# Optimization experiments

Measured on AMD Instinct MI355X. Metric: run time of the kernel, lower is better.

## Reference

```python
import jax, jax.numpy as jnp
import numpy as np

# ---- fixed architecture constants (hard-coded in Wavenet_Barebones.__init__) ----
B = 2
T_FRAMES = 64
UPS = (4, 4, 4, 4)
T = T_FRAMES * 256            # 16384 audio samples
VOCAB = 259
CH = 128
CC = 80                       # conditioning (mel) channels
K = 3                         # dilated conv kernel size
LAYERS = 24
LAYERS_PER_STACK = 6          # 24 // 4
FC1 = 512


def setup_inputs() -> dict:
    key = jax.random.key(0)
    ks = iter(jax.random.split(key, 32))
    nrm = lambda shape, s: jax.random.normal(next(ks), shape, jnp.float32) * s
    return {
        "x": jax.random.randint(next(ks), (B, T), 0, VOCAB),          # mu-law token ids
        "c": jax.random.normal(next(ks), (B, CC, T_FRAMES), jnp.float32),  # mel frames (B,C,Tf)
        "emb": nrm((VOCAB, CH), 1.0),
        "enc_w": nrm((CH, CH), 0.08), "enc_b": jnp.zeros((CH,), jnp.float32),
        "conv_w": nrm((LAYERS, CH, CH, K), 0.05),  # (L, out, in, k)
        "conv_b": jnp.zeros((LAYERS, CH), jnp.float32),
        "cond_w": nrm((LAYERS, CH, CC), 0.05),     # per-layer 1x1 local-conditioning proj
        "cond_b": jnp.zeros((LAYERS, CH), jnp.float32),
        "fc1_w": nrm((FC1, CH), 0.08), "fc1_b": jnp.zeros((FC1,), jnp.float32),
        "fc2_w": nrm((VOCAB, FC1), 0.04), "fc2_b": jnp.zeros((VOCAB,), jnp.float32),
        "ups_w": nrm((4, 3, 4), 0.3),              # 4 ConvTranspose2d kernels (freq=3, time=4)
        "ups_b": jnp.zeros((4,), jnp.float32),
    }


def _upsample(c, ups_w, ups_b):
    """r9y9 UpsampleNetwork: stack of ConvTranspose2d(1,1,(3,s),stride=(1,s),padding=(1,0)) + ReLU.
    c: (B, CC, Tf) -> (B, CC, Tf*256)."""
    y = c[:, None]  # (B, 1, CC, Tf)
    for i, s in enumerate(UPS):
        # transposed conv == input dilation by s + correlation with spatially-flipped kernel
        w = ups_w[i][::-1, ::-1][None, None]  # (O=1, I=1, 3, s)
        y = jax.lax.conv_general_dilated(
            y, w, window_strides=(1, 1),
            padding=[(1, 1), (s - 1, s - 1)],   # freq: kh-1-pad=1; time: kw-1-0=s-1
            lhs_dilation=(1, s),
            dimension_numbers=("NCHW", "OIHW", "NCHW"))
        y = jax.nn.relu(y + ups_b[i])
    return y[:, 0]  # (B, CC, T)


def reference(x, c, emb, enc_w, enc_b, conv_w, conv_b, cond_w, cond_b,
              fc1_w, fc1_b, fc2_w, fc2_b, ups_w, ups_b):
    # encode: embedding -> relu(linear)   (dropout is inference-disabled)
    h = jax.nn.relu(jnp.einsum("btc,oc->bto", emb[x], enc_w) + enc_b)  # (B,T,CH)
    cu = _upsample(c, ups_w, ups_b)                                     # (B,CC,T)
    h = h.transpose(0, 2, 1)                                            # (B,CH,T)
    dn = ("NCH", "OIH", "NCH")
    for l in range(LAYERS):
        d = 2 ** (l % LAYERS_PER_STACK)
        p = (K - 1) * d  # causal left pad
        y = jax.lax.conv_general_dilated(
            h, conv_w[l], window_strides=(1,), padding=[(p, 0)],
            rhs_dilation=(d,), dimension_numbers=dn)
        y = jax.nn.relu(y + conv_b[l][:, None])
        cond = jnp.einsum("oc,bct->bot", cond_w[l], cu) + cond_b[l][:, None]
        h = jax.nn.relu(y + cond + h)  # conditioning + residual, outer F.relu from forward loop
    h = h.transpose(0, 2, 1)                                            # (B,T,CH)
    h = jax.nn.relu(jnp.einsum("btc,oc->bto", h, fc1_w) + fc1_b)
    out = jnp.einsum("btf,of->bto", h, fc2_w) + fc2_b                   # (B,T,VOCAB)
    return out[:, :-1, :]
```

## Files before the change

kernel.cpp:

```cpp
#include <hip/hip_runtime.h>

typedef __bf16 bf16;
typedef __attribute__((ext_vector_type(8))) __bf16 bf16x8;
typedef __attribute__((ext_vector_type(4))) __bf16 bf16x4;
typedef __attribute__((ext_vector_type(4))) float f32x4;

namespace {
constexpr int Bn = 2;
constexpr int T  = 16384;
constexpr int NL = 24;
constexpr int VOC = 259;
}

#define MFMA_B16(a, b, c) __builtin_amdgcn_mfma_f32_16x16x32_bf16((a), (b), (c), 0, 0, 0)

__global__ void prep_wconv_k(const float* __restrict__ cw, const float* __restrict__ dw,
                             bf16* __restrict__ W2) {
  int total = NL * 61440;
  for (int idx = blockIdx.x * 256 + threadIdx.x; idx < total; idx += gridDim.x * 256) {
    int l = idx / 61440; int r = idx % 61440;
    int s = r >> 12; int of = (r >> 9) & 7; int lane = (r >> 3) & 63; int j = r & 7;
    int o = of * 16 + (lane & 15);
    int kk = (lane >> 4) * 8 + j;
    float v;
    if (s < 12) { int k = s >> 2; int c = (s & 3) * 32 + kk; v = cw[((l * 128 + o) * 128 + c) * 3 + k]; }
    else        { int cc = (s - 12) * 32 + kk; v = (cc < 80) ? dw[(l * 128 + o) * 80 + cc] : 0.f; }
    W2[idx] = (bf16)v;
  }
}

__global__ void prep_misc_k(const float* __restrict__ fc1w, const float* __restrict__ encw,
                            const float* __restrict__ emb, const float* __restrict__ fc2w,
                            bf16* __restrict__ fc1wb, bf16* __restrict__ encwb,
                            bf16* __restrict__ embb, bf16* __restrict__ w2f) {
  const int n1 = 65536, n2 = 16384, n3 = 33152, n4 = 196608;
  int total = n1 + n2 + n3 + n4;
  for (int idx = blockIdx.x * 256 + threadIdx.x; idx < total; idx += gridDim.x * 256) {
    if (idx < n1) { fc1wb[idx] = (bf16)fc1w[idx]; }
    else if (idx < n1 + n2) { int i = idx - n1; encwb[i] = (bf16)encw[i]; }
    else if (idx < n1 + n2 + n3) { int i = idx - n1 - n2; embb[i] = (bf16)emb[i]; }
    else {
      int r = idx - n1 - n2 - n3;
      int s = r / 12288; int r2 = r % 12288;
      int ot = r2 >> 9; int lane = (r2 >> 3) & 63; int j = r2 & 7;
      int o = ot * 16 + (lane & 15);
      int f = s * 32 + (lane >> 4) * 8 + j;
      w2f[r] = (bf16)((o < VOC) ? fc2w[o * 512 + f] : 0.f);
    }
  }
}

__global__ void ups_stage_k(const float* __restrict__ in, float* __restrict__ out,
                            const float* __restrict__ W, const float* __restrict__ bptr, int Win) {
  int Wout = Win * 4;
  int total = Bn * 80 * Wout;
  float bias = *bptr;
  for (int idx = blockIdx.x * 256 + threadIdx.x; idx < total; idx += gridDim.x * 256) {
    int w = idx % Wout; int rest = idx / Wout;
    int hrow = rest % 80; int b = rest / 80;
    int win = w >> 2; int kw = w & 3;
    float acc = bias;
#pragma unroll
    for (int kh = 0; kh < 3; ++kh) {
      int hr = hrow + 1 - kh;
      if (hr >= 0 && hr < 80) acc += in[(b * 80 + hr) * Win + win] * W[kh * 4 + kw];
    }
    out[idx] = fmaxf(acc, 0.f);
  }
}

__global__ void ups4_cuT_k(const float* __restrict__ in, const float* __restrict__ W,
                           const float* __restrict__ bptr, bf16* __restrict__ cuT2) {
  int total = Bn * 1024 * 3 * 512;
  float bias = *bptr;
  for (int idx = blockIdx.x * 256 + threadIdx.x; idx < total; idx += gridDim.x * 256) {
    int low = idx & 511; int j = low & 7; int lane = low >> 3;
    int g = idx >> 9; int sc = g % 3; int gt = g / 3; int tile = gt & 1023; int b = gt >> 10;
    int lr = lane & 15, lk = lane >> 4;
    int t = tile * 16 + lr;
    int cc = sc * 32 + lk * 8 + j;
    float v = 0.f;
    if (cc < 80) {
      int win = t >> 2, kw = t & 3;
      float acc = bias;
#pragma unroll
      for (int kh = 0; kh < 3; ++kh) {
        int hr = cc + 1 - kh;
        if (hr >= 0 && hr < 80) acc += in[(b * 80 + hr) * 4096 + win] * W[kh * 4 + kw];
      }
      v = fmaxf(acc, 0.f);
    }
    cuT2[idx] = (bf16)v;
  }
}

__global__ __launch_bounds__(256, 2) void encode_k(
    const int* __restrict__ x, const bf16* __restrict__ embb, const bf16* __restrict__ encwb,
    const float* __restrict__ encb, bf16* __restrict__ hbt) {
  __shared__ char Eb[16384];
  int t0 = blockIdx.x * 64, b = blockIdx.y;
  int tid = threadIdx.x, lane = tid & 63, wid = tid >> 6, wr = wid >> 1, wc = wid & 1;
  int lr = lane & 15, lk = lane >> 4;
  int tb = t0 + wc * 32;
  int xi[2];
#pragma unroll
  for (int n = 0; n < 2; ++n) xi[n] = x[b * T + tb + n * 16 + lr];
  f32x4 acc[4][2] = {};
#pragma unroll
  for (int s = 0; s < 4; ++s) {
    bf16x8 a[4], bb[2];
#pragma unroll
    for (int m = 0; m < 4; ++m) a[m] = *(const bf16x8*)(encwb + (wr * 64 + m * 16 + lr) * 128 + s * 32 + lk * 8);
#pragma unroll
    for (int n = 0; n < 2; ++n) bb[n] = *(const bf16x8*)(embb + xi[n] * 128 + s * 32 + lk * 8);
#pragma unroll
    for (int m = 0; m < 4; ++m)
#pragma unroll
      for (int n = 0; n < 2; ++n) acc[m][n] = MFMA_B16(a[m], bb[n], acc[m][n]);
  }
#pragma unroll
  for (int m = 0; m < 4; ++m)
#pragma unroll
    for (int n = 0; n < 2; ++n) {
      int obase = wr * 64 + m * 16 + lk * 4;
      int row = wc * 32 + n * 16 + lr;
      bf16x4 p;
#pragma unroll
      for (int r = 0; r < 4; ++r) p[r] = (bf16)fmaxf(acc[m][n][r] + encb[obase + r], 0.f);
      int byteo = obase * 2;
      int slot = ((byteo >> 4) ^ (row & 7)) & 15;
      *(bf16x4*)(Eb + row * 256 + (slot << 4) + (byteo & 15)) = p;
    }
  __syncthreads();
  const size_t btb = (size_t)b * T;
  for (int u = tid; u < 1024; u += 256) {
    int row = u >> 4, slot = u & 15;
    uint4 v = *(const uint4*)(Eb + row * 256 + ((((slot) ^ (row & 7)) & 15) << 4));
    *(uint4*)(hbt + (btb + t0 + row) * 128 + slot * 8) = v;
  }
}

template <int D1>
__global__ __launch_bounds__(512, 4) void layer2_k(
    const bf16* __restrict__ hbt_in, bf16* __restrict__ hbt_out,
    const bf16* __restrict__ W2, const bf16* __restrict__ cuT2,
    const float* __restrict__ cb1, const float* __restrict__ db1,
    const float* __restrict__ cb2, const float* __restrict__ db2) {
  constexpr int D2 = 2 * D1;
  constexpr int EXT = (D1 == 16) ? 64 : 16;
  constexpr int NMF = EXT / 16;
  constexpr int NF = NMF + 4;
  constexpr int NCH = (D1 == 16) ? 2 : 1;
  constexpr int NFC = NF / NCH;
  constexpr int AOFF = EXT + 2 * D1;
  constexpr int AR = 64 + AOFF;
  constexpr int BR = 64 + EXT;
  __shared__ uint4 Au[AR * 16];
  __shared__ uint4 Bu[BR * 16];
  char* AB = (char*)Au;
  char* BB = (char*)Bu;
  const int bx = blockIdx.x;
  const int tblk = ((bx & 7) << 5) | (bx >> 3);
  const int t0 = tblk * 64, b = blockIdx.y;
  const int tid = threadIdx.x, lane = tid & 63, wid = tid >> 6;
  const int lr = lane & 15, lk = lane >> 4;
  const size_t btb = (size_t)b * T;
  const size_t bt16 = (size_t)b * 1024;
  const bf16* Wa = W2;
  const bf16* Wb = W2 + 61440;

  uint4 zv; zv.x = zv.y = zv.z = zv.w = 0;
  for (int u = tid; u < AR * 16; u += 512) {
    int row = u >> 4, slot = u & 15;
    int t = t0 - AOFF + row;
    uint4 v = (t >= 0) ? *(const uint4*)(hbt_in + (btb + t) * 128 + slot * 8) : zv;
    *(uint4*)(AB + row * 256 + (((slot ^ (row & 7)) & 15) << 4)) = v;
  }
  __syncthreads();

  f32x4 hl[4];
  const int ob = wid * 16 + lk * 4;
  const f32x4 dv1 = *(const f32x4*)(db1 + ob);
  const int byteo = ob * 2, slot0 = byteo >> 4, wib = byteo & 15;
#pragma unroll
  for (int ch = 0; ch < NCH; ++ch) {
    const int fb = ch * NFC;
    f32x4 acc[NFC] = {};
#pragma unroll
    for (int s = 0; s < 12; ++s) {
      const int k = s >> 2, shift = (k - 2) * D1, sb = (s & 3) * 4;
      bf16x8 a = *(const bf16x8*)(Wa + ((s * 8 + wid) * 64 + lane) * 8);
#pragma unroll
      for (int n = 0; n < NFC; ++n) {
        int row = 2 * D1 + (fb + n) * 16 + lr + shift;
        int slot = ((sb + lk) ^ (row & 7)) & 15;
        bf16x8 bb = *(const bf16x8*)(AB + row * 256 + slot * 16);
        acc[n] = MFMA_B16(a, bb, acc[n]);
      }
    }
    {
      const f32x4 bv = *(const f32x4*)(cb1 + wid * 16 + lk * 4);
#pragma unroll
      for (int n = 0; n < NFC; ++n)
#pragma unroll
        for (int r = 0; r < 4; ++r) acc[n][r] = fmaxf(acc[n][r] + bv[r], 0.f);
    }
#pragma unroll
    for (int s = 12; s < 15; ++s) {
      bf16x8 a = *(const bf16x8*)(Wa + ((s * 8 + wid) * 64 + lane) * 8);
#pragma unroll
      for (int n = 0; n < NFC; ++n) {
        int tb2 = t0 - EXT + (fb + n) * 16;
        int tile = (tb2 < 0 ? 0 : tb2) >> 4;
        bf16x8 bb = *(const bf16x8*)(cuT2 + ((bt16 + tile) * 3 + (s - 12)) * 512 + lane * 8);
        acc[n] = MFMA_B16(a, bb, acc[n]);
      }
    }
#pragma unroll
    for (int n = 0; n < NFC; ++n) {
      const int gn = fb + n;
      const int t = t0 - EXT + gn * 16 + lr;
      const int rowA = 2 * D1 + gn * 16 + lr;
      const int slotA = (slot0 ^ (rowA & 7)) & 15;
      bf16x4 hb = *(const bf16x4*)(AB + rowA * 256 + (slotA << 4) + wib);
      bf16x4 p;
#pragma unroll
      for (int r = 0; r < 4; ++r) {
        float vv = fmaxf(acc[n][r] + dv1[r] + (float)hb[r], 0.f);
        if (t < 0) vv = 0.f;
        if (gn >= NMF) hl[gn - NMF][r] = vv;
        p[r] = (bf16)vv;
      }
      const int rb = gn * 16 + lr;
      *(bf16x4*)(BB + rb * 256 + (((slot0 ^ (rb & 7)) & 15) << 4) + wib) = p;
    }
  }
  __syncthreads();

  f32x4 a2[4] = {};
#pragma unroll
  for (int s = 0; s < 12; ++s) {
    const int k = s >> 2, shift = (k - 2) * D2, sb = (s & 3) * 4;
    bf16x8 a = *(const bf16x8*)(Wb + ((s * 8 + wid) * 64 + lane) * 8);
#pragma unroll
    for (int n = 0; n < 4; ++n) {
      int row = EXT + n * 16 + lr + shift;
      int slot = ((sb + lk) ^ (row & 7)) & 15;
      bf16x8 bb = *(const bf16x8*)(BB + row * 256 + slot * 16);
      a2[n] = MFMA_B16(a, bb, a2[n]);
    }
  }
  {
    const f32x4 bv = *(const f32x4*)(cb2 + wid * 16 + lk * 4);
#pragma unroll
    for (int n = 0; n < 4; ++n)
#pragma unroll
      for (int r = 0; r < 4; ++r) a2[n][r] = fmaxf(a2[n][r] + bv[r], 0.f);
  }
#pragma unroll
  for (int s = 12; s < 15; ++s) {
    bf16x8 a = *(const bf16x8*)(Wb + ((s * 8 + wid) * 64 + lane) * 8);
#pragma unroll
    for (int n = 0; n < 4; ++n) {
      int tile = (t0 + n * 16) >> 4;
      bf16x8 bb = *(const bf16x8*)(cuT2 + ((bt16 + tile) * 3 + (s - 12)) * 512 + lane * 8);
      a2[n] = MFMA_B16(a, bb, a2[n]);
    }
  }
  const f32x4 dv2 = *(const f32x4*)(db2 + ob);
  bf16x4 po[4];
#pragma unroll
  for (int n = 0; n < 4; ++n)
#pragma unroll
    for (int r = 0; r < 4; ++r)
      po[n][r] = (bf16)fmaxf(a2[n][r] + dv2[r] + hl[n][r], 0.f);
  __syncthreads();
#pragma unroll
  for (int n = 0; n < 4; ++n) {
    const int rb = n * 16 + lr;
    *(bf16x4*)(BB + rb * 256 + (((slot0 ^ (rb & 7)) & 15) << 4) + wib) = po[n];
  }
  __syncthreads();
  for (int u = tid; u < 1024; u += 512) {
    int row = u >> 4, slot = u & 15;
    uint4 v = *(const uint4*)(BB + row * 256 + (((slot ^ (row & 7)) & 15) << 4));
    *(uint4*)(hbt_out + (btb + t0 + row) * 128 + slot * 8) = v;
  }
}

__global__ __launch_bounds__(512, 4) void fc1_k(
    const bf16* __restrict__ hbt, const bf16* __restrict__ fc1wb,
    const float* __restrict__ b1, bf16* __restrict__ a1f) {
  __shared__ char H[16384];
  int t0 = blockIdx.x * 64, b = blockIdx.y;
  int tid = threadIdx.x, lane = tid & 63, wid = tid >> 6;
  int lr = lane & 15, lk = lane >> 4;
  const size_t btb = (size_t)b * T;
  for (int u = tid; u < 1024; u += 512) {
    int row = u >> 4, slot = u & 15;
    uint4 v = *(const uint4*)(hbt + (btb + t0 + row) * 128 + slot * 8);
    *(uint4*)(H + row * 256 + (((slot ^ (row & 7)) & 15) << 4)) = v;
  }
  __syncthreads();
  int wf = wid >> 1, wc = wid & 1;
#pragma unroll
  for (int f0 = 0; f0 < 2; ++f0) {
    f32x4 acc[4][2] = {};
#pragma unroll
    for (int s = 0; s < 4; ++s) {
      bf16x8 a[4], bb[2];
#pragma unroll
      for (int m = 0; m < 4; ++m)
        a[m] = *(const bf16x8*)(fc1wb + (f0 * 256 + wf * 64 + m * 16 + lr) * 128 + s * 32 + lk * 8);
#pragma unroll
      for (int n = 0; n < 2; ++n) {
        int row = wc * 32 + n * 16 + lr;
        int slot = ((s * 4 + lk) ^ (row & 7)) & 15;
        bb[n] = *(const bf16x8*)(H + row * 256 + slot * 16);
      }
#pragma unroll
      for (int m = 0; m < 4; ++m)
#pragma unroll
        for (int n = 0; n < 2; ++n) acc[m][n] = MFMA_B16(a[m], bb[n], acc[m][n]);
    }
#pragma unroll
    for (int m = 0; m < 4; ++m) {
      int fb = f0 * 256 + wf * 64 + m * 16 + lk * 4;
      const f32x4 bv = *(const f32x4*)(b1 + fb);
      int lhi = (fb >> 3) & 3, j0 = fb & 7, s16 = fb >> 5;
#pragma unroll
      for (int n = 0; n < 2; ++n) {
        int t = t0 + wc * 32 + n * 16 + lr;
        bf16x4 p;
#pragma unroll
        for (int r = 0; r < 4; ++r) p[r] = (bf16)fmaxf(acc[m][n][r] + bv[r], 0.f);
        size_t addr = (((size_t)b * 1024 + (t >> 4)) * 16 + s16) * 512 + (lhi * 16 + (t & 15)) * 8 + j0;
        *(bf16x4*)(a1f + addr) = p;
      }
    }
  }
}

__global__ __launch_bounds__(512, 4) void fc2_k(
    const bf16* __restrict__ a1f, const bf16* __restrict__ w2f,
    const float* __restrict__ b2, float* __restrict__ out) {
  int t0 = blockIdx.x * 64, b = blockIdx.y;
  int tid = threadIdx.x, lane = tid & 63, wid = tid >> 6;
  int lr = lane & 15, lk = lane >> 4;
  const size_t tb16 = (size_t)b * 1024 + (t0 >> 4);
  f32x4 acc[4][3] = {};
#pragma unroll 4
  for (int s = 0; s < 16; ++s) {
    bf16x8 a[4], bb[3];
#pragma unroll
    for (int mt = 0; mt < 4; ++mt)
      a[mt] = *(const bf16x8*)(a1f + ((tb16 + mt) * 16 + s) * 512 + lane * 8);
#pragma unroll
    for (int no = 0; no < 3; ++no)
      bb[no] = *(const bf16x8*)(w2f + ((s * 24 + wid * 3 + no) * 64 + lane) * 8);
#pragma unroll
    for (int mt = 0; mt < 4; ++mt)
#pragma unroll
      for (int no = 0; no < 3; ++no) acc[mt][no] = MFMA_B16(a[mt], bb[no], acc[mt][no]);
  }
#pragma unroll
  for (int mt = 0; mt < 4; ++mt)
#pragma unroll
    for (int no = 0; no < 3; ++no) {
      int o = (wid * 3 + no) * 16 + lr;
      if (o >= VOC) continue;
      float bias = b2[o];
#pragma unroll
      for (int r = 0; r < 4; ++r) {
        int tg = t0 + mt * 16 + lk * 4 + r;
        if (tg < T - 1) out[((size_t)b * (T - 1) + tg) * VOC + o] = acc[mt][no][r] + bias;
      }
    }
}

extern "C" void kernel_launch(void* const* d_in, const int* in_sizes, int n_in,
                              void* d_out, int out_size, void* d_ws, size_t ws_size,
                              hipStream_t stream) {
  const int*   x      = (const int*)d_in[0];
  const float* c      = (const float*)d_in[1];
  const float* emb    = (const float*)d_in[2];
  const float* enc_w  = (const float*)d_in[3];
  const float* enc_b  = (const float*)d_in[4];
  const float* conv_w = (const float*)d_in[5];
  const float* conv_b = (const float*)d_in[6];
  const float* cond_w = (const float*)d_in[7];
  const float* cond_b = (const float*)d_in[8];
  const float* fc1_w  = (const float*)d_in[9];
  const float* fc1_b  = (const float*)d_in[10];
  const float* fc2_w  = (const float*)d_in[11];
  const float* fc2_b  = (const float*)d_in[12];
  const float* ups_w  = (const float*)d_in[13];
  const float* ups_b  = (const float*)d_in[14];
  float* out = (float*)d_out;
  (void)in_sizes; (void)n_in; (void)out_size; (void)ws_size;

  char* w = (char*)d_ws;
  bf16* hbtA  = (bf16*)w;  w += 8388608;
  bf16* hbtB  = (bf16*)w;  w += 8388608;
  bf16* cuT2  = (bf16*)w;  w += 6291456;
  bf16* W2    = (bf16*)w;  w += 2949120;
  bf16* fc1wb = (bf16*)w;  w += 131072;
  bf16* encwb = (bf16*)w;  w += 32768;
  bf16* embb  = (bf16*)w;  w += 66560;
  bf16* w2f   = (bf16*)w;  w += 393216;
  bf16* a1f   = (bf16*)w;  w += 33554432;
  float* u1   = (float*)w; w += 2621440;
  float* u2   = (float*)w; w += 655360;

  prep_wconv_k<<<dim3(2880), dim3(256), 0, stream>>>(conv_w, cond_w, W2);
  prep_misc_k<<<dim3(1218), dim3(256), 0, stream>>>(fc1_w, enc_w, emb, fc2_w, fc1wb, encwb, embb, w2f);

  ups_stage_k<<<dim3(160),  dim3(256), 0, stream>>>(c,  u1, ups_w + 0,  ups_b + 0, 64);
  ups_stage_k<<<dim3(640),  dim3(256), 0, stream>>>(u1, u2, ups_w + 12, ups_b + 1, 256);
  ups_stage_k<<<dim3(2560), dim3(256), 0, stream>>>(u2, u1, ups_w + 24, ups_b + 2, 1024);
  ups4_cuT_k<<<dim3(4096),  dim3(256), 0, stream>>>(u1, ups_w + 36, ups_b + 3, cuT2);

  encode_k<<<dim3(T / 64, Bn), dim3(256), 0, stream>>>(x, embb, encwb, enc_b, hbtA);

  bf16* hti = hbtA; bf16* hto = hbtB;
  for (int p = 0; p < 12; ++p) {
    int d1 = 1 << ((2 * p) % 6);
    const bf16* wl = W2 + (size_t)p * 2 * 61440;
    const float* cb1 = conv_b + (2 * p) * 128;
    const float* db1 = cond_b + (2 * p) * 128;
    const float* cb2 = conv_b + (2 * p + 1) * 128;
    const float* db2 = cond_b + (2 * p + 1) * 128;
    dim3 g(T / 64, Bn);
    switch (d1) {
      case 1:  layer2_k<1><<<g,  dim3(512), 0, stream>>>(hti, hto, wl, cuT2, cb1, db1, cb2, db2); break;
      case 4:  layer2_k<4><<<g,  dim3(512), 0, stream>>>(hti, hto, wl, cuT2, cb1, db1, cb2, db2); break;
      case 16: layer2_k<16><<<g, dim3(512), 0, stream>>>(hti, hto, wl, cuT2, cb1, db1, cb2, db2); break;
    }
    bf16* t1 = hti; hti = hto; hto = t1;
  }

  fc1_k<<<dim3(T / 64, Bn), dim3(512), 0, stream>>>(hti, fc1wb, fc1_b, a1f);
  fc2_k<<<dim3(T / 64, Bn), dim3(512), 0, stream>>>(a1f, w2f, fc2_b, out);
}
```

Baseline: 297.4 us.

## Remap layer2 warps to 32x32 output tiles to share B fragments across two MFMAs

Changes the warp-to-tile mapping in the fused two-layer dilated conv kernel. Each warp previously covered 16 output channels across all time tiles; it now covers 32 output channels across every other time tile. Each LDS B-fragment load then feeds two MFMAs, which cuts shared-memory traffic per MFMA in half. The cost is two weight A-fragments loaded per step, and a less even workload when the number of time tiles is odd, since rg==1 warps skip a tile.

```diff
diff --git a/kernel.cpp b/kernel.cpp
--- a/kernel.cpp
+++ b/kernel.cpp
@@ -150,8 +150,9 @@
   constexpr int EXT = (D1 == 16) ? 64 : 16;
   constexpr int NMF = EXT / 16;
   constexpr int NF = NMF + 4;
+  constexpr int NIMAX = (NF + 1) / 2;
   constexpr int NCH = (D1 == 16) ? 2 : 1;
-  constexpr int NFC = NF / NCH;
+  constexpr int NIC = NIMAX / NCH;
   constexpr int AOFF = EXT + 2 * D1;
   constexpr int AR = 64 + AOFF;
   constexpr int BR = 64 + EXT;
@@ -163,6 +164,7 @@
   const int tblk = ((bx & 7) << 5) | (bx >> 3);
   const int t0 = tblk * 64, b = blockIdx.y;
   const int tid = threadIdx.x, lane = tid & 63, wid = tid >> 6;
+  const int og = wid >> 1, rg = wid & 1;
   const int lr = lane & 15, lk = lane >> 4;
   const size_t btb = (size_t)b * T;
   const size_t bt16 = (size_t)b * 1024;
@@ -178,107 +180,150 @@
   }
   __syncthreads();
 
-  f32x4 hl[4];
-  const int ob = wid * 16 + lk * 4;
-  const f32x4 dv1 = *(const f32x4*)(db1 + ob);
-  const int byteo = ob * 2, slot0 = byteo >> 4, wib = byteo & 15;
+  f32x4 hl[2][2];
+  const int ob0 = og * 32 + lk * 4;
+  const f32x4 dv1a = *(const f32x4*)(db1 + ob0);
+  const f32x4 dv1b = *(const f32x4*)(db1 + ob0 + 16);
+  const f32x4 cv1a = *(const f32x4*)(cb1 + ob0);
+  const f32x4 cv1b = *(const f32x4*)(cb1 + ob0 + 16);
 #pragma unroll
   for (int ch = 0; ch < NCH; ++ch) {
-    const int fb = ch * NFC;
-    f32x4 acc[NFC] = {};
+    f32x4 acc[2][NIC] = {};
 #pragma unroll
     for (int s = 0; s < 12; ++s) {
       const int k = s >> 2, shift = (k - 2) * D1, sb = (s & 3) * 4;
-      bf16x8 a = *(const bf16x8*)(Wa + ((s * 8 + wid) * 64 + lane) * 8);
-#pragma unroll
-      for (int n = 0; n < NFC; ++n) {
-        int row = 2 * D1 + (fb + n) * 16 + lr + shift;
-        int slot = ((sb + lk) ^ (row & 7)) & 15;
-        bf16x8 bb = *(const bf16x8*)(AB + row * 256 + slot * 16);
-        acc[n] = MFMA_B16(a, bb, acc[n]);
-      }
-    }
-    {
-      const f32x4 bv = *(const f32x4*)(cb1 + wid * 16 + lk * 4);
-#pragma unroll
-      for (int n = 0; n < NFC; ++n)
-#pragma unroll
-        for (int r = 0; r < 4; ++r) acc[n][r] = fmaxf(acc[n][r] + bv[r], 0.f);
-    }
+      bf16x8 a0 = *(const bf16x8*)(Wa + ((s * 8 + og * 2) * 64 + lane) * 8);
+      bf16x8 a1 = *(const bf16x8*)(Wa + ((s * 8 + og * 2 + 1) * 64 + lane) * 8);
+#pragma unroll
+      for (int i = 0; i < NIC; ++i) {
+        const int idx = ch * NIC + i;
+        if (2 * idx + 1 < NF || rg == 0) {
+          const int gn = 2 * idx + rg;
+          int row = 2 * D1 + gn * 16 + lr + shift;
+          int slot = ((sb + lk) ^ (row & 7)) & 15;
+          bf16x8 bb = *(const bf16x8*)(AB + row * 256 + slot * 16);
+          acc[0][i] = MFMA_B16(a0, bb, acc[0][i]);
+          acc[1][i] = MFMA_B16(a1, bb, acc[1][i]);
+        }
+      }
+    }
+#pragma unroll
+    for (int i = 0; i < NIC; ++i)
+#pragma unroll
+      for (int r = 0; r < 4; ++r) {
+        acc[0][i][r] = fmaxf(acc[0][i][r] + cv1a[r], 0.f);
+        acc[1][i][r] = fmaxf(acc[1][i][r] + cv1b[r], 0.f);
+      }
 #pragma unroll
     for (int s = 12; s < 15; ++s) {
-      bf16x8 a = *(const bf16x8*)(Wa + ((s * 8 + wid) * 64 + lane) * 8);
-#pragma unroll
-      for (int n = 0; n < NFC; ++n) {
-        int tb2 = t0 - EXT + (fb + n) * 16;
-        int tile = (tb2 < 0 ? 0 : tb2) >> 4;
-        bf16x8 bb = *(const bf16x8*)(cuT2 + ((bt16 + tile) * 3 + (s - 12)) * 512 + lane * 8);
-        acc[n] = MFMA_B16(a, bb, acc[n]);
-      }
-    }
-#pragma unroll
-    for (int n = 0; n < NFC; ++n) {
-      const int gn = fb + n;
-      const int t = t0 - EXT + gn * 16 + lr;
-      const int rowA = 2 * D1 + gn * 16 + lr;
-      const int slotA = (slot0 ^ (rowA & 7)) & 15;
-      bf16x4 hb = *(const bf16x4*)(AB + rowA * 256 + (slotA << 4) + wib);
-      bf16x4 p;
-#pragma unroll
-      for (int r = 0; r < 4; ++r) {
-        float vv = fmaxf(acc[n][r] + dv1[r] + (float)hb[r], 0.f);
-        if (t < 0) vv = 0.f;
-        if (gn >= NMF) hl[gn - NMF][r] = vv;
-        p[r] = (bf16)vv;
-      }
-      const int rb = gn * 16 + lr;
-      *(bf16x4*)(BB + rb * 256 + (((slot0 ^ (rb & 7)) & 15) << 4) + wib) = p;
-    }
-  }
-  __syncthreads();
-
-  f32x4 a2[4] = {};
+      bf16x8 a0 = *(const bf16x8*)(Wa + ((s * 8 + og * 2) * 64 + lane) * 8);
+      bf16x8 a1 = *(const bf16x8*)(Wa + ((s * 8 + og * 2 + 1) * 64 + lane) * 8);
+#pragma unroll
+      for (int i = 0; i < NIC; ++i) {
+        const int idx = ch * NIC + i;
+        if (2 * idx + 1 < NF || rg == 0) {
+          const int gn = 2 * idx + rg;
+          int tb2 = t0 - EXT + gn * 16;
+          int tile = (tb2 < 0 ? 0 : tb2) >> 4;
+          bf16x8 bb = *(const bf16x8*)(cuT2 + ((bt16 + tile) * 3 + (s - 12)) * 512 + lane * 8);
+          acc[0][i] = MFMA_B16(a0, bb, acc[0][i]);
+          acc[1][i] = MFMA_B16(a1, bb, acc[1][i]);
+        }
+      }
+    }
+#pragma unroll
+    for (int i = 0; i < NIC; ++i) {
+      const int idx = ch * NIC + i;
+      if (2 * idx + 1 < NF || rg == 0) {
+        const int gn = 2 * idx + rg;
+        const int t = t0 - EXT + gn * 16 + lr;
+        const int rowA = 2 * D1 + gn * 16 + lr;
+        const int rb = gn * 16 + lr;
+#pragma unroll
+        for (int which = 0; which < 2; ++which) {
+          const int byteo = (ob0 + which * 16) * 2;
+          const int slot0 = byteo >> 4, wib = byteo & 15;
+          const int slotA = (slot0 ^ (rowA & 7)) & 15;
+          bf16x4 hb = *(const bf16x4*)(AB + rowA * 256 + (slotA << 4) + wib);
+          const f32x4 dv = which ? dv1b : dv1a;
+          bf16x4 p;
+#pragma unroll
+          for (int r = 0; r < 4; ++r) {
+            float vv = fmaxf(acc[which][i][r] + dv[r] + (float)hb[r], 0.f);
+            if (t < 0) vv = 0.f;
+            if (gn >= NMF) hl[which][(gn - NMF) >> 1][r] = vv;
+            p[r] = (bf16)vv;
+          }
+          *(bf16x4*)(BB + rb * 256 + (((slot0 ^ (rb & 7)) & 15) << 4) + wib) = p;
+        }
+      }
+    }
+  }
+  __syncthreads();
+
+  const int n0 = (rg + NMF) & 1;
+  f32x4 a2[2][2] = {};
 #pragma unroll
   for (int s = 0; s < 12; ++s) {
     const int k = s >> 2, shift = (k - 2) * D2, sb = (s & 3) * 4;
-    bf16x8 a = *(const bf16x8*)(Wb + ((s * 8 + wid) * 64 + lane) * 8);
-#pragma unroll
-    for (int n = 0; n < 4; ++n) {
+    bf16x8 a0 = *(const bf16x8*)(Wb + ((s * 8 + og * 2) * 64 + lane) * 8);
+    bf16x8 a1 = *(const bf16x8*)(Wb + ((s * 8 + og * 2 + 1) * 64 + lane) * 8);
+#pragma unroll
+    for (int mi = 0; mi < 2; ++mi) {
+      const int n = n0 + 2 * mi;
       int row = EXT + n * 16 + lr + shift;
       int slot = ((sb + lk) ^ (row & 7)) & 15;
       bf16x8 bb = *(const bf16x8*)(BB + row * 256 + slot * 16);
-      a2[n] = MFMA_B16(a, bb, a2[n]);
+      a2[0][mi] = MFMA_B16(a0, bb, a2[0][mi]);
+      a2[1][mi] = MFMA_B16(a1, bb, a2[1][mi]);
     }
   }
   {
-    const f32x4 bv = *(const f32x4*)(cb2 + wid * 16 + lk * 4);
-#pragma unroll
-    for (int n = 0; n < 4; ++n)
-#pragma unroll
-      for (int r = 0; r < 4; ++r) a2[n][r] = fmaxf(a2[n][r] + bv[r], 0.f);
+    const f32x4 cv2a = *(const f32x4*)(cb2 + ob0);
+    const f32x4 cv2b = *(const f32x4*)(cb2 + ob0 + 16);
+#pragma unroll
+    for (int mi = 0; mi < 2; ++mi)
+#pragma unroll
+      for (int r = 0; r < 4; ++r) {
+        a2[0][mi][r] = fmaxf(a2[0][mi][r] + cv2a[r], 0.f);
+        a2[1][mi][r] = fmaxf(a2[1][mi][r] + cv2b[r], 0.f);
+      }
   }
 #pragma unroll
   for (int s = 12; s < 15; ++s) {
-    bf16x8 a = *(const bf16x8*)(Wb + ((s * 8 + wid) * 64 + lane) * 8);
-#pragma unroll
-    for (int n = 0; n < 4; ++n) {
+    bf16x8 a0 = *(const bf16x8*)(Wb + ((s * 8 + og * 2) * 64 + lane) * 8);
+    bf16x8 a1 = *(const bf16x8*)(Wb + ((s * 8 + og * 2 + 1) * 64 + lane) * 8);
+#pragma unroll
+    for (int mi = 0; mi < 2; ++mi) {
+      const int n = n0 + 2 * mi;
       int tile = (t0 + n * 16) >> 4;
       bf16x8 bb = *(const bf16x8*)(cuT2 + ((bt16 + tile) * 3 + (s - 12)) * 512 + lane * 8);
-      a2[n] = MFMA_B16(a, bb, a2[n]);
-    }
-  }
-  const f32x4 dv2 = *(const f32x4*)(db2 + ob);
-  bf16x4 po[4];
-#pragma unroll
-  for (int n = 0; n < 4; ++n)
-#pragma unroll
-    for (int r = 0; r < 4; ++r)
-      po[n][r] = (bf16)fmaxf(a2[n][r] + dv2[r] + hl[n][r], 0.f);
-  __syncthreads();
-#pragma unroll
-  for (int n = 0; n < 4; ++n) {
-    const int rb = n * 16 + lr;
-    *(bf16x4*)(BB + rb * 256 + (((slot0 ^ (rb & 7)) & 15) << 4) + wib) = po[n];
+      a2[0][mi] = MFMA_B16(a0, bb, a2[0][mi]);
+      a2[1][mi] = MFMA_B16(a1, bb, a2[1][mi]);
+    }
+  }
+  const f32x4 dv2a = *(const f32x4*)(db2 + ob0);
+  const f32x4 dv2b = *(const f32x4*)(db2 + ob0 + 16);
+  bf16x4 po[2][2];
+#pragma unroll
+  for (int which = 0; which < 2; ++which) {
+    const f32x4 dv = which ? dv2b : dv2a;
+#pragma unroll
+    for (int mi = 0; mi < 2; ++mi)
+#pragma unroll
+      for (int r = 0; r < 4; ++r)
+        po[which][mi][r] = (bf16)fmaxf(a2[which][mi][r] + dv[r] + hl[which][mi][r], 0.f);
+  }
+  __syncthreads();
+#pragma unroll
+  for (int mi = 0; mi < 2; ++mi) {
+    const int rb = (n0 + 2 * mi) * 16 + lr;
+#pragma unroll
+    for (int which = 0; which < 2; ++which) {
+      const int byteo = (ob0 + which * 16) * 2;
+      const int slot0 = byteo >> 4, wib = byteo & 15;
+      *(bf16x4*)(BB + rb * 256 + (((slot0 ^ (rb & 7)) & 15) << 4) + wib) = po[which][mi];
+    }
   }
   __syncthreads();
   for (int u = tid; u < 1024; u += 512) {
```

New measurement: 312.1 us. 4.9% more time.
